# Kernel optimization log

Measured on AMD Instinct MI355X. Metric: run time of the kernel, lower is better.

## Reference

```python
import jax, jax.numpy as jnp
import numpy as np
import math

HIDDEN_DIM = 1024
NUM_HEADS = 16
HEAD_DIM = HIDDEN_DIM // NUM_HEADS  # 64

def setup_inputs() -> dict:
    key = jax.random.key(0)
    k1, k2, k3 = jax.random.split(key, 3)
    x = jax.random.normal(k1, (8, 4096, HIDDEN_DIM), dtype=jnp.float32)
    W = jax.random.normal(k2, (HIDDEN_DIM, NUM_HEADS), dtype=jnp.float32) * (1.0 / math.sqrt(HIDDEN_DIM))
    mask = jax.random.randint(k3, (8, 4096), 0, 2, dtype=jnp.int32)
    return {"x": x, "W": W, "mask": mask}

def reference(x, W, mask):
    B, S, D = x.shape
    # linear scoring: [B,S,H], scaled by sqrt(head_dim)
    logits = jnp.einsum('bsd,dh->bsh', x, W) / math.sqrt(HEAD_DIM)
    # mask out padded positions (mask==0 -> -inf) before softmax over seq axis
    logits = jnp.where(mask[:, :, None] == 0, -jnp.inf, logits)
    attn = jax.nn.softmax(logits, axis=1)  # softmax over sequence dim
    # dropout is identity in eval mode
    # weighted sum: original expands x over heads, so each head pools the full hidden vector
    pooled = jnp.einsum('bsh,bsd->bhd', attn, x)  # [B, H, D]
    return pooled.reshape(B, NUM_HEADS * D)
```

## Files before the change

### kernel.cpp

```cpp
#include <hip/hip_runtime.h>
#include <math.h>

#define BB 8
#define SS 4096
#define DD 1024
#define HH 16

typedef __attribute__((ext_vector_type(4))) float f32x4;
typedef __fp16 fp16x2 __attribute__((ext_vector_type(2)));
typedef _Float16 half8v __attribute__((ext_vector_type(8)));


__device__ __forceinline__ void sm_merge(float& m, float& z, float om, float oz) {
  float nm = fmaxf(m, om);
  if (nm > -INFINITY)
    z = z * __expf(m - nm) + oz * __expf(om - nm);
  m = nm;
}

__global__ __launch_bounds__(256) void k_prepw(
    const float* __restrict__ W, ushort* __restrict__ wh16, ushort* __restrict__ wl16) {
  int i = blockIdx.x * 256 + threadIdx.x;
  int t = i >> 9;
  int l = (i >> 3) & 63;
  int e = i & 7;
  int d = t * 32 + (l >> 4) * 8 + e;
  int h = l & 15;
  float w = W[d * HH + h];
  _Float16 wh = (_Float16)w;
  _Float16 wl = (_Float16)(w - (float)wh);
  union { _Float16 f; ushort u; } ch, cl;
  ch.f = wh; cl.f = wl;
  wh16[i] = ch.u;
  wl16[i] = cl.u;
}

__global__ __launch_bounds__(256, 4) void k_logits(
    const float* __restrict__ x, const ushort* __restrict__ wh16,
    const ushort* __restrict__ wl16, float* __restrict__ plog) {
  __shared__ float4 lds4[2][4][16][16];

  const int tid = threadIdx.x;
  const int lane = tid & 63;
  const int wv = tid >> 6;
  const int kh = blockIdx.x & 1;
  const int tile = blockIdx.x >> 1;
  const int b = tile >> 6;
  const int s0 = (tile & 63) * 64;
  const int r15 = lane & 15;
  const int kg = lane >> 4;
  const int srow = lane >> 4;
  const int sul = lane & 15;

  const float* xw = x + ((size_t)b * SS + s0 + wv * 16) * DD + kh * 512;
  const half8v* bhp = reinterpret_cast<const half8v*>(wh16) + (kh * 16 * 64 + lane);
  const half8v* blp = reinterpret_cast<const half8v*>(wl16) + (kh * 16 * 64 + lane);

  f32x4 acch = {0.f, 0.f, 0.f, 0.f};
  f32x4 accl = {0.f, 0.f, 0.f, 0.f};

  float4 stA[4], stB[4];
  half8v whc[2], wlc[2], whn[2], wln[2];

#pragma unroll
  for (int k = 0; k < 4; ++k) {
    int row = k * 4 + srow;
    stA[k] = *reinterpret_cast<const float4*>(xw + (size_t)row * DD + sul * 4);
  }
#pragma unroll
  for (int j = 0; j < 2; ++j) { whc[j] = bhp[j * 64]; wlc[j] = blp[j * 64]; }
#pragma unroll
  for (int k = 0; k < 4; ++k) {
    int row = k * 4 + srow;
    lds4[0][wv][row][sul ^ (row & 7)] = stA[k];
  }
#pragma unroll
  for (int k = 0; k < 4; ++k) {
    int row = k * 4 + srow;
    stB[k] = *reinterpret_cast<const float4*>(xw + (size_t)row * DD + 64 + sul * 4);
  }

#pragma unroll
  for (int c = 0; c < 8; ++c) {
    if (c < 6) {
      float4* stN = ((c & 1) == 0) ? stA : stB;
#pragma unroll
      for (int k = 0; k < 4; ++k) {
        int row = k * 4 + srow;
        stN[k] = *reinterpret_cast<const float4*>(
            xw + (size_t)row * DD + (c + 2) * 64 + sul * 4);
      }
    }
    if (c < 7) {
#pragma unroll
      for (int j = 0; j < 2; ++j) {
        whn[j] = bhp[((c + 1) * 2 + j) * 64];
        wln[j] = blp[((c + 1) * 2 + j) * 64];
      }
    }

#pragma unroll
    for (int t4 = 0; t4 < 2; ++t4) {
      const int u0 = t4 * 8 + kg * 2;
      float4 va = lds4[c & 1][wv][r15][u0 ^ (r15 & 7)];
      float4 vb = lds4[c & 1][wv][r15][(u0 + 1) ^ (r15 & 7)];
      union { fp16x2 h2[4]; half8v h8; } ax;
      ax.h2[0] = __builtin_amdgcn_cvt_pkrtz(va.x, va.y);
      ax.h2[1] = __builtin_amdgcn_cvt_pkrtz(va.z, va.w);
      ax.h2[2] = __builtin_amdgcn_cvt_pkrtz(vb.x, vb.y);
      ax.h2[3] = __builtin_amdgcn_cvt_pkrtz(vb.z, vb.w);
      acch = __builtin_amdgcn_mfma_f32_16x16x32_f16(ax.h8, whc[t4], acch, 0, 0, 0);
      accl = __builtin_amdgcn_mfma_f32_16x16x32_f16(ax.h8, wlc[t4], accl, 0, 0, 0);
    }

    if (c < 7) {
      float4* stW = (((c + 1) & 1) == 0) ? stA : stB;
#pragma unroll
      for (int k = 0; k < 4; ++k) {
        int row = k * 4 + srow;
        lds4[(c + 1) & 1][wv][row][sul ^ (row & 7)] = stW[k];
      }
      whc[0] = whn[0]; whc[1] = whn[1];
      wlc[0] = wln[0]; wlc[1] = wln[1];
    }
  }

  float* ob = plog + (size_t)kh * (BB * SS * HH) +
              ((size_t)b * SS + s0 + wv * 16) * HH;
#pragma unroll
  for (int q = 0; q < 4; ++q)
    ob[(size_t)(kg * 4 + q) * HH + r15] = acch[q] + accl[q];
}

__global__ __launch_bounds__(256) void k_smpart(
    const float* __restrict__ plog, const int* __restrict__ mask,
    float2* __restrict__ bred) {
  __shared__ float4 smm[4][4], smz[4][4];
  const int tid = threadIdx.x;
  const int lane = tid & 63;
  const int wv = tid >> 6;
  const int b = blockIdx.x >> 5;
  const int sc = blockIdx.x & 31;
  const int s0 = sc * 128;
  const float4* p0 = reinterpret_cast<const float4*>(plog + ((size_t)b * SS + s0) * HH);
  const float4* p1 = reinterpret_cast<const float4*>(
      plog + (size_t)BB * SS * HH + ((size_t)b * SS + s0) * HH);
  const int* mb = mask + b * SS + s0;

  float m4[4] = {-INFINITY, -INFINITY, -INFINITY, -INFINITY};
  float z4[4] = {0.f, 0.f, 0.f, 0.f};
#pragma unroll
  for (int i = 0; i < 2; ++i) {
    int f = i * 256 + tid;
    float4 va = p0[f];
    float4 vb = p1[f];
    int msk = mb[f >> 2];
    float lv[4] = {(va.x + vb.x) * 0.125f, (va.y + vb.y) * 0.125f,
                   (va.z + vb.z) * 0.125f, (va.w + vb.w) * 0.125f};
#pragma unroll
    for (int j = 0; j < 4; ++j) {
      float v = msk ? lv[j] : -INFINITY;
      sm_merge(m4[j], z4[j], v, 1.0f);
    }
  }
#pragma unroll
  for (int off = 4; off < 64; off <<= 1) {
#pragma unroll
    for (int j = 0; j < 4; ++j) {
      float om = __shfl_xor(m4[j], off, 64);
      float oz = __shfl_xor(z4[j], off, 64);
      sm_merge(m4[j], z4[j], om, oz);
    }
  }
  if (lane < 4) {
    smm[wv][lane] = make_float4(m4[0], m4[1], m4[2], m4[3]);
    smz[wv][lane] = make_float4(z4[0], z4[1], z4[2], z4[3]);
  }
  __syncthreads();
  if (tid < 4) {
    float4 mm = smm[0][tid], zz = smz[0][tid];
    float fm[4] = {mm.x, mm.y, mm.z, mm.w};
    float fz[4] = {zz.x, zz.y, zz.z, zz.w};
#pragma unroll
    for (int w = 1; w < 4; ++w) {
      float4 om4 = smm[w][tid], oz4 = smz[w][tid];
      float om[4] = {om4.x, om4.y, om4.z, om4.w};
      float oz[4] = {oz4.x, oz4.y, oz4.z, oz4.w};
#pragma unroll
      for (int j = 0; j < 4; ++j) sm_merge(fm[j], fz[j], om[j], oz[j]);
    }
#pragma unroll
    for (int j = 0; j < 4; ++j)
      bred[((size_t)b * 32 + sc) * HH + tid * 4 + j] = make_float2(fm[j], fz[j]);
  }
}

__global__ __launch_bounds__(256) void k_pool(
    const float* __restrict__ x, const float* __restrict__ plog,
    const float2* __restrict__ bred, const int* __restrict__ mask,
    float* __restrict__ partial) {
  __shared__ float wl[128][16];
  __shared__ float fm[16], fz[16];
  const int tid = threadIdx.x;
  const int dh = blockIdx.x & 1;
  const int sc = (blockIdx.x >> 1) & 31;
  const int b = blockIdx.x >> 6;
  const int s0 = sc * 128;

  if (tid < 16) {
    float m = -INFINITY, z = 0.f;
#pragma unroll 4
    for (int c = 0; c < 32; ++c) {
      float2 p = bred[((size_t)b * 32 + c) * HH + tid];
      sm_merge(m, z, p.x, p.y);
    }
    fm[tid] = m;
    fz[tid] = (z > 0.f) ? 1.0f / z : 0.f;
  }
  __syncthreads();

  const float4* p0 = reinterpret_cast<const float4*>(plog + ((size_t)b * SS + s0) * HH);
  const float4* p1 = reinterpret_cast<const float4*>(
      plog + (size_t)BB * SS * HH + ((size_t)b * SS + s0) * HH);
  const int* mb = mask + b * SS + s0;
#pragma unroll
  for (int k = 0; k < 2; ++k) {
    int f = k * 256 + tid;
    float4 va = p0[f];
    float4 vb = p1[f];
    int msk = mb[f >> 2];
    int hb = (f & 3) * 4;
    float4 w;
    w.x = msk ? __expf((va.x + vb.x) * 0.125f - fm[hb + 0]) * fz[hb + 0] : 0.f;
    w.y = msk ? __expf((va.y + vb.y) * 0.125f - fm[hb + 1]) * fz[hb + 1] : 0.f;
    w.z = msk ? __expf((va.z + vb.z) * 0.125f - fm[hb + 2]) * fz[hb + 2] : 0.f;
    w.w = msk ? __expf((va.w + vb.w) * 0.125f - fm[hb + 3]) * fz[hb + 3] : 0.f;
    *reinterpret_cast<float4*>(&wl[0][0] + f * 4) = w;
  }
  __syncthreads();

  float2 acc[HH];
#pragma unroll
  for (int h = 0; h < HH; ++h) acc[h] = make_float2(0.f, 0.f);

  const float* xb = x + ((size_t)b * SS + s0) * DD + dh * 512 + tid * 2;
  for (int s = 0; s < 128; ++s) {
    float2 xv = *reinterpret_cast<const float2*>(xb + (size_t)s * DD);
    const float4* wrow = reinterpret_cast<const float4*>(wl[s]);
    float4 wa = wrow[0], wb_ = wrow[1], wc = wrow[2], wd = wrow[3];
    float wvv[16] = {wa.x, wa.y, wa.z, wa.w, wb_.x, wb_.y, wb_.z, wb_.w,
                     wc.x, wc.y, wc.z, wc.w, wd.x, wd.y, wd.z, wd.w};
#pragma unroll
    for (int h = 0; h < HH; ++h) {
      float w = wvv[h];
      acc[h].x += w * xv.x;
      acc[h].y += w * xv.y;
    }
  }

  float* pb = partial + ((size_t)sc * BB + b) * (HH * DD) + dh * 512 + tid * 2;
#pragma unroll
  for (int h = 0; h < HH; ++h)
    *reinterpret_cast<float2*>(pb + (size_t)h * DD) = acc[h];
}

__global__ __launch_bounds__(256) void k_reduce(
    const float* __restrict__ partial, float* __restrict__ out) {
  const int idx = blockIdx.x * 256 + threadIdx.x;
  float s = 0.f;
#pragma unroll
  for (int c = 0; c < 32; ++c) s += partial[(size_t)c * (BB * HH * DD) + idx];
  out[idx] = s;
}

extern "C" void kernel_launch(void* const* d_in, const int* in_sizes, int n_in,
                              void* d_out, int out_size, void* d_ws, size_t ws_size,
                              hipStream_t stream) {
  const float* x = (const float*)d_in[0];
  const float* W = (const float*)d_in[1];
  const int* mask = (const int*)d_in[2];
  float* out = (float*)d_out;

  char* ws = (char*)d_ws;
  float* plog    = (float*)ws;
  float* partial = (float*)(ws + (size_t)6 * 1024 * 1024);
  ushort* wh16   = (ushort*)(ws + (size_t)22 * 1024 * 1024);
  ushort* wl16   = (ushort*)(ws + (size_t)22 * 1024 * 1024 + 32 * 1024);
  float2* bred   = (float2*)(ws + (size_t)23 * 1024 * 1024);

  k_prepw<<<64, 256, 0, stream>>>(W, wh16, wl16);
  k_logits<<<1024, 256, 0, stream>>>(x, wh16, wl16, plog);
  k_smpart<<<256, 256, 0, stream>>>(plog, mask, bred);
  k_pool<<<512, 256, 0, stream>>>(x, plog, bred, mask, partial);
  k_reduce<<<512, 256, 0, stream>>>(partial, out);
}
```

Baseline: 74.96 us.

## Stage x tiles via direct global-to-LDS loads and halve pool sequence splits

The logits kernel now uses global_load_lds to copy x chunks straight into LDS, with explicit vmcnt/lgkmcnt waits and double-buffered weight fragments. This replaces the register-staged loads and ds_write stores, cutting VGPR pressure and instruction count. Separately, the pooling kernel covers 256 sequence positions per block instead of 128, which halves the partial-sum buffer and the reduce work but leaves only 256 blocks and therefore less parallelism. The hand-written waitcnt values depend on the compiler's instruction ordering and could be fragile.

New measurement: 91.28 us. 1.22x slower.

```diff
diff --git a/kernel.cpp b/kernel.cpp
--- a/kernel.cpp
+++ b/kernel.cpp
@@ -35,6 +35,14 @@
   wl16[i] = cl.u;
 }
 
+__device__ __forceinline__ void stage_chunk(const float* const* gsrc, char* lb, int c) {
+#pragma unroll
+  for (int k = 0; k < 4; ++k)
+    __builtin_amdgcn_global_load_lds(
+        (const __attribute__((address_space(1))) void*)(gsrc[k] + c * 64),
+        (__attribute__((address_space(3))) void*)(lb + k * 1024), 16, 0, 0);
+}
+
 __global__ __launch_bounds__(256, 4) void k_logits(
     const float* __restrict__ x, const ushort* __restrict__ wh16,
     const ushort* __restrict__ wl16, float* __restrict__ plog) {
@@ -42,62 +50,44 @@
 
   const int tid = threadIdx.x;
   const int lane = tid & 63;
-  const int wv = tid >> 6;
+  const int wv = __builtin_amdgcn_readfirstlane(tid >> 6);
   const int kh = blockIdx.x & 1;
   const int tile = blockIdx.x >> 1;
   const int b = tile >> 6;
   const int s0 = (tile & 63) * 64;
   const int r15 = lane & 15;
   const int kg = lane >> 4;
-  const int srow = lane >> 4;
-  const int sul = lane & 15;
 
   const float* xw = x + ((size_t)b * SS + s0 + wv * 16) * DD + kh * 512;
   const half8v* bhp = reinterpret_cast<const half8v*>(wh16) + (kh * 16 * 64 + lane);
   const half8v* blp = reinterpret_cast<const half8v*>(wl16) + (kh * 16 * 64 + lane);
 
+  const float* gsrc[4];
+#pragma unroll
+  for (int k = 0; k < 4; ++k) {
+    int row = k * 4 + (lane >> 4);
+    int u = (lane & 15) ^ (row & 7);
+    gsrc[k] = xw + (size_t)row * DD + u * 4;
+  }
+
   f32x4 acch = {0.f, 0.f, 0.f, 0.f};
   f32x4 accl = {0.f, 0.f, 0.f, 0.f};
-
-  float4 stA[4], stB[4];
-  half8v whc[2], wlc[2], whn[2], wln[2];
-
-#pragma unroll
-  for (int k = 0; k < 4; ++k) {
-    int row = k * 4 + srow;
-    stA[k] = *reinterpret_cast<const float4*>(xw + (size_t)row * DD + sul * 4);
-  }
-#pragma unroll
-  for (int j = 0; j < 2; ++j) { whc[j] = bhp[j * 64]; wlc[j] = blp[j * 64]; }
-#pragma unroll
-  for (int k = 0; k < 4; ++k) {
-    int row = k * 4 + srow;
-    lds4[0][wv][row][sul ^ (row & 7)] = stA[k];
-  }
-#pragma unroll
-  for (int k = 0; k < 4; ++k) {
-    int row = k * 4 + srow;
-    stB[k] = *reinterpret_cast<const float4*>(xw + (size_t)row * DD + 64 + sul * 4);
-  }
+  half8v whf[2][2], wlf[2][2];
+
+  char* lb0 = (char*)&lds4[0][wv][0][0];
+  char* lb1 = (char*)&lds4[1][wv][0][0];
+
+  stage_chunk(gsrc, lb0, 0);
+  whf[0][0] = bhp[0 * 64]; whf[0][1] = bhp[1 * 64];
+  wlf[0][0] = blp[0 * 64]; wlf[0][1] = blp[1 * 64];
+  stage_chunk(gsrc, lb1, 1);
+  whf[1][0] = bhp[2 * 64]; whf[1][1] = bhp[3 * 64];
+  wlf[1][0] = blp[2 * 64]; wlf[1][1] = blp[3 * 64];
 
 #pragma unroll
   for (int c = 0; c < 8; ++c) {
-    if (c < 6) {
-      float4* stN = ((c & 1) == 0) ? stA : stB;
-#pragma unroll
-      for (int k = 0; k < 4; ++k) {
-        int row = k * 4 + srow;
-        stN[k] = *reinterpret_cast<const float4*>(
-            xw + (size_t)row * DD + (c + 2) * 64 + sul * 4);
-      }
-    }
-    if (c < 7) {
-#pragma unroll
-      for (int j = 0; j < 2; ++j) {
-        whn[j] = bhp[((c + 1) * 2 + j) * 64];
-        wln[j] = blp[((c + 1) * 2 + j) * 64];
-      }
-    }
+    if (c < 7) asm volatile("s_waitcnt vmcnt(8)" ::: "memory");
+    else       asm volatile("s_waitcnt vmcnt(0)" ::: "memory");
 
 #pragma unroll
     for (int t4 = 0; t4 < 2; ++t4) {
@@ -109,19 +99,17 @@
       ax.h2[1] = __builtin_amdgcn_cvt_pkrtz(va.z, va.w);
       ax.h2[2] = __builtin_amdgcn_cvt_pkrtz(vb.x, vb.y);
       ax.h2[3] = __builtin_amdgcn_cvt_pkrtz(vb.z, vb.w);
-      acch = __builtin_amdgcn_mfma_f32_16x16x32_f16(ax.h8, whc[t4], acch, 0, 0, 0);
-      accl = __builtin_amdgcn_mfma_f32_16x16x32_f16(ax.h8, wlc[t4], accl, 0, 0, 0);
-    }
-
-    if (c < 7) {
-      float4* stW = (((c + 1) & 1) == 0) ? stA : stB;
-#pragma unroll
-      for (int k = 0; k < 4; ++k) {
-        int row = k * 4 + srow;
-        lds4[(c + 1) & 1][wv][row][sul ^ (row & 7)] = stW[k];
-      }
-      whc[0] = whn[0]; whc[1] = whn[1];
-      wlc[0] = wln[0]; wlc[1] = wln[1];
+      acch = __builtin_amdgcn_mfma_f32_16x16x32_f16(ax.h8, whf[c & 1][t4], acch, 0, 0, 0);
+      accl = __builtin_amdgcn_mfma_f32_16x16x32_f16(ax.h8, wlf[c & 1][t4], accl, 0, 0, 0);
+    }
+
+    if (c < 6) {
+      asm volatile("s_waitcnt lgkmcnt(0)" ::: "memory");
+      stage_chunk(gsrc, (c & 1) ? lb1 : lb0, c + 2);
+      whf[c & 1][0] = bhp[(2 * (c + 2) + 0) * 64];
+      whf[c & 1][1] = bhp[(2 * (c + 2) + 1) * 64];
+      wlf[c & 1][0] = blp[(2 * (c + 2) + 0) * 64];
+      wlf[c & 1][1] = blp[(2 * (c + 2) + 1) * 64];
     }
   }
 
@@ -199,13 +187,13 @@
     const float* __restrict__ x, const float* __restrict__ plog,
     const float2* __restrict__ bred, const int* __restrict__ mask,
     float* __restrict__ partial) {
-  __shared__ float wl[128][16];
+  __shared__ float wl[256][16];
   __shared__ float fm[16], fz[16];
   const int tid = threadIdx.x;
   const int dh = blockIdx.x & 1;
-  const int sc = (blockIdx.x >> 1) & 31;
-  const int b = blockIdx.x >> 6;
-  const int s0 = sc * 128;
+  const int sc = (blockIdx.x >> 1) & 15;
+  const int b = blockIdx.x >> 5;
+  const int s0 = sc * 256;
 
   if (tid < 16) {
     float m = -INFINITY, z = 0.f;
@@ -224,7 +212,7 @@
       plog + (size_t)BB * SS * HH + ((size_t)b * SS + s0) * HH);
   const int* mb = mask + b * SS + s0;
 #pragma unroll
-  for (int k = 0; k < 2; ++k) {
+  for (int k = 0; k < 4; ++k) {
     int f = k * 256 + tid;
     float4 va = p0[f];
     float4 vb = p1[f];
@@ -244,7 +232,8 @@
   for (int h = 0; h < HH; ++h) acc[h] = make_float2(0.f, 0.f);
 
   const float* xb = x + ((size_t)b * SS + s0) * DD + dh * 512 + tid * 2;
-  for (int s = 0; s < 128; ++s) {
+#pragma unroll 8
+  for (int s = 0; s < 256; ++s) {
     float2 xv = *reinterpret_cast<const float2*>(xb + (size_t)s * DD);
     const float4* wrow = reinterpret_cast<const float4*>(wl[s]);
     float4 wa = wrow[0], wb_ = wrow[1], wc = wrow[2], wd = wrow[3];
@@ -269,7 +258,7 @@
   const int idx = blockIdx.x * 256 + threadIdx.x;
   float s = 0.f;
 #pragma unroll
-  for (int c = 0; c < 32; ++c) s += partial[(size_t)c * (BB * HH * DD) + idx];
+  for (int c = 0; c < 16; ++c) s += partial[(size_t)c * (BB * HH * DD) + idx];
   out[idx] = s;
 }
 
@@ -291,6 +280,6 @@
   k_prepw<<<64, 256, 0, stream>>>(W, wh16, wl16);
   k_logits<<<1024, 256, 0, stream>>>(x, wh16, wl16, plog);
   k_smpart<<<256, 256, 0, stream>>>(plog, mask, bred);
-  k_pool<<<512, 256, 0, stream>>>(x, plog, bred, mask, partial);
+  k_pool<<<256, 256, 0, stream>>>(x, plog, bred, mask, partial);
   k_reduce<<<512, 256, 0, stream>>>(partial, out);
 }
```
